# Optimization experiments

Measured on AMD Instinct MI355X. Metric: run time of the kernel, lower is better.

Reference implementation:

```python
import jax, jax.numpy as jnp
import numpy as np

X_DIM, Z_DIM, H, B, T = 257, 16, 128, 256, 512


def _p(key, shape, scale=0.05):
    return jax.random.normal(key, shape, jnp.float32) * scale


def setup_inputs() -> dict:
    key = jax.random.key(0)
    ks = jax.random.split(key, 16)
    z4 = jnp.zeros((4 * H,), jnp.float32)
    return {
        "x": jax.random.uniform(ks[0], (B, X_DIM, T), jnp.float32),
        "eps": jax.random.normal(ks[1], (T, B, Z_DIM), jnp.float32),
        # rnn_g_x: backward LSTM over x
        "Wih_gx": _p(ks[2], (4 * H, X_DIM)), "Whh_gx": _p(ks[3], (4 * H, H)),
        "bih_gx": z4, "bhh_gx": z4,
        # rnn_g_z: forward LSTM cell over sampled z
        "Wih_gz": _p(ks[4], (4 * H, Z_DIM)), "Whh_gz": _p(ks[5], (4 * H, H)),
        "bih_gz": z4, "bhh_gz": z4,
        # mlp_inference (one dense layer, tanh) + heads
        "W0": _p(ks[6], (H, 2 * H)), "b0": jnp.zeros((H,), jnp.float32),
        "Wm": _p(ks[7], (Z_DIM, H)), "bm": jnp.zeros((Z_DIM,), jnp.float32),
        "Wv": _p(ks[8], (Z_DIM, H)), "bv": jnp.zeros((Z_DIM,), jnp.float32),
        # decoder rnn_h + gen_logvar
        "Wih_h": _p(ks[9], (4 * H, Z_DIM)), "Whh_h": _p(ks[10], (4 * H, H)),
        "bih_h": z4, "bhh_h": z4,
        "Wy": _p(ks[11], (X_DIM, H)), "by": jnp.zeros((X_DIM,), jnp.float32),
    }


def _lstm(xs, Wih, Whh, b, reverse=False):
    # xs: (T, B, in); single-layer LSTM, PyTorch gate order i,f,g,o
    Bn, Hd = xs.shape[1], Whh.shape[1]

    def step(carry, x_t):
        h, c = carry
        g = x_t @ Wih.T + h @ Whh.T + b
        i, f, gg, o = jnp.split(g, 4, axis=-1)
        c = jax.nn.sigmoid(f) * c + jax.nn.sigmoid(i) * jnp.tanh(gg)
        h = jax.nn.sigmoid(o) * jnp.tanh(c)
        return (h, c), h

    init = (jnp.zeros((Bn, Hd), xs.dtype), jnp.zeros((Bn, Hd), xs.dtype))
    _, hs = jax.lax.scan(step, init, xs, reverse=reverse)
    return hs


def reference(x, eps, Wih_gx, Whh_gx, bih_gx, bhh_gx,
              Wih_gz, Whh_gz, bih_gz, bhh_gz,
              W0, b0, Wm, bm, Wv, bv,
              Wih_h, Whh_h, bih_h, bhh_h, Wy, by):
    xt = jnp.transpose(x, (2, 0, 1))  # (T, B, x_dim)
    # g_x = flip(LSTM(flip(x))) == backward-direction LSTM
    g_x = _lstm(xt, Wih_gx, Whh_gx, bih_gx + bhh_gx, reverse=True)
    bz = bih_gz + bhh_gz
    Hz = Whh_gz.shape[1]

    def inf_step(carry, inp):
        g_z, c_z = carry  # hidden of rnn_g_z BEFORE seeing current z
        gx_t, eps_t = inp
        h = jnp.tanh(jnp.concatenate([gx_t, g_z], axis=-1) @ W0.T + b0)
        mean = h @ Wm.T + bm
        logvar = h @ Wv.T + bv
        z_t = eps_t * jnp.exp(0.5 * logvar) + mean  # reparameterize
        # one LSTM-cell step of rnn_g_z on z_t (used at next timestep)
        g = z_t @ Wih_gz.T + g_z @ Whh_gz.T + bz
        i, f, gg, o = jnp.split(g, 4, axis=-1)
        c_z = jax.nn.sigmoid(f) * c_z + jax.nn.sigmoid(i) * jnp.tanh(gg)
        g_z = jax.nn.sigmoid(o) * jnp.tanh(c_z)
        return (g_z, c_z), (mean, logvar, z_t)

    Bn = xt.shape[1]
    init = (jnp.zeros((Bn, Hz), x.dtype), jnp.zeros((Bn, Hz), x.dtype))
    _, (mean, logvar, z) = jax.lax.scan(inf_step, init, (g_x, eps))
    # generation
    hdec = _lstm(z, Wih_h, Whh_h, bih_h + bhh_h)
    y = jnp.exp(hdec @ Wy.T + by)  # (T, B, x_dim)
    perm = lambda a: jnp.transpose(a, (1, 2, 0))  # -> (B, dim, T)
    return perm(y), perm(mean), perm(logvar), perm(z)
```

## Files before the change

### kernel.cpp

```cpp
#include <hip/hip_runtime.h>
#include <stdint.h>

#define T_SEQ 512
#define BATCH 256
#define HID   128
#define G4    512
#define XD    257
#define ZD    16

__device__ __forceinline__ float bf2f(uint16_t u) {
  union { uint32_t i; float f; } v; v.i = ((uint32_t)u) << 16; return v.f;
}
__device__ __forceinline__ uint16_t f2bf(float f) {
  union { float f; uint32_t i; } v; v.f = f;
  uint32_t r = v.i + 0x7fffu + ((v.i >> 16) & 1u);
  return (uint16_t)(r >> 16);
}
__device__ __forceinline__ float sigf(float x) { return 1.0f / (1.0f + __expf(-x)); }
__device__ __forceinline__ float tanhfast(float x) { return 2.0f / (1.0f + __expf(-2.0f * x)) - 1.0f; }
__device__ __forceinline__ float gate_act(float pre, bool isg) {
  float s = isg ? (-2.0f * pre) : (-pre);
  float r = 1.0f / (1.0f + __expf(s));
  return isg ? (2.0f * r - 1.0f) : r;
}

__global__ void k_prep(const float* __restrict__ Wih_gx, const float* __restrict__ Wy,
                       float* __restrict__ wT, float* __restrict__ wyT) {
  int idx = blockIdx.x * 256 + threadIdx.x;
  const int N1 = XD * G4;
  const int N2 = HID * XD;
  if (idx < N1) {
    int j = idx & (G4 - 1), d = idx >> 9;
    wT[idx] = Wih_gx[j * XD + d];
  } else if (idx < N1 + N2) {
    int i2 = idx - N1;
    int u = i2 / XD, d = i2 % XD;
    wyT[i2] = Wy[d * HID + u];
  }
}

__global__ __launch_bounds__(256) void k_proj(
    const float* __restrict__ x, const float* __restrict__ wT,
    const float* __restrict__ bih, const float* __restrict__ bhh,
    uint16_t* __restrict__ px) {
  __shared__ uint16_t xs[XD * 66];
  int tid = threadIdx.x;
  int t0 = blockIdx.x * 64, b = blockIdx.y;
  int lane = tid & 63;
  {
    int t = tid & 63, d0 = tid >> 6;
    for (int d = d0; d < XD; d += 4)
      xs[d * 66 + t] = f2bf(x[((size_t)b * XD + d) * T_SEQ + t0 + t]);
  }
  __syncthreads();
  int w = __builtin_amdgcn_readfirstlane(tid >> 6);
  for (int p = 0; p < 8; ++p) {
    int j0 = w * 128 + p * 16;
    float acc[16];
#pragma unroll
    for (int i = 0; i < 16; ++i) acc[i] = bih[j0 + i] + bhh[j0 + i];
    for (int d = 0; d < XD; ++d) {
      float xv = bf2f(xs[d * 66 + lane]);
      const float* wrow = wT + (size_t)d * G4 + j0;
#pragma unroll
      for (int i = 0; i < 16; ++i) acc[i] = fmaf(wrow[i], xv, acc[i]);
    }
    size_t base = ((size_t)(t0 + lane) * BATCH + b) * G4 + j0;
    uint32_t pk[8];
#pragma unroll
    for (int i = 0; i < 8; ++i)
      pk[i] = (uint32_t)f2bf(acc[2 * i]) | ((uint32_t)f2bf(acc[2 * i + 1]) << 16);
    uint4* dst = (uint4*)(px + base);
    dst[0] = make_uint4(pk[0], pk[1], pk[2], pk[3]);
    dst[1] = make_uint4(pk[4], pk[5], pk[6], pk[7]);
  }
}

__global__ __launch_bounds__(512, 2) void k_lstm_gx(
    const uint16_t* __restrict__ px, const float* __restrict__ Whh,
    uint16_t* __restrict__ gx) {
  __shared__ __align__(16) float hl[2][HID];
  int tid = threadIdx.x, b = blockIdx.x;
  int u = tid >> 2, g = tid & 3;
  int j = g * HID + u;
  float wr[HID];
#pragma unroll
  for (int k = 0; k < HID; ++k) wr[k] = Whh[(size_t)j * HID + k];
  if (tid < HID) hl[0][tid] = 0.0f;
  float c = 0.0f;
  int cur = 0;
  int ql = (tid & 63) & ~3;
  bool isg = (g == 2);
  uint16_t pcur = px[((size_t)(T_SEQ - 1) * BATCH + b) * G4 + j];
  __syncthreads();
  for (int t = T_SEQ - 1; t >= 0; --t) {
    int tn = t > 0 ? t - 1 : 0;
    uint16_t pnext = px[((size_t)tn * BATCH + b) * G4 + j];
    float pre = bf2f(pcur);
    const float4* h4 = (const float4*)hl[cur];
#pragma unroll
    for (int k4 = 0; k4 < HID / 4; ++k4) {
      float4 h = h4[k4];
      pre = fmaf(wr[4 * k4 + 0], h.x, pre);
      pre = fmaf(wr[4 * k4 + 1], h.y, pre);
      pre = fmaf(wr[4 * k4 + 2], h.z, pre);
      pre = fmaf(wr[4 * k4 + 3], h.w, pre);
    }
    float act = gate_act(pre, isg);
    float af = __shfl(act, ql + 1);
    float ag = __shfl(act, ql + 2);
    float ao = __shfl(act, ql + 3);
    if (g == 0) {
      c = af * c + act * ag;
      float h = ao * tanhfast(c);
      hl[cur ^ 1][u] = h;
      gx[((size_t)t * BATCH + b) * HID + u] = f2bf(h);
    }
    cur ^= 1;
    pcur = pnext;
    __syncthreads();
  }
}

__global__ __launch_bounds__(512, 2) void k_inf(
    const uint16_t* __restrict__ gx, const float* __restrict__ eps,
    const float* __restrict__ Wih_gz, const float* __restrict__ Whh_gz,
    const float* __restrict__ bih_gz, const float* __restrict__ bhh_gz,
    const float* __restrict__ W0, const float* __restrict__ b0,
    const float* __restrict__ Wm, const float* __restrict__ bm,
    const float* __restrict__ Wv, const float* __restrict__ bv,
    float* __restrict__ zbuf, float* __restrict__ out_mean,
    float* __restrict__ out_logvar, float* __restrict__ out_z) {
  __shared__ float wgzT2[ZD * 512];
  __shared__ __align__(16) float gxl[HID];
  __shared__ __align__(16) float gzl[2][HID];
  __shared__ __align__(16) float hvec[HID];
  __shared__ __align__(16) float zl[ZD];
  int tid = threadIdx.x, b = blockIdx.x;
  int u = tid >> 2, g = tid & 3;
  int j = g * HID + u;
#pragma unroll
  for (int k = 0; k < ZD; ++k) wgzT2[k * 512 + tid] = Wih_gz[(size_t)j * ZD + k];
  float wzr[HID];
#pragma unroll
  for (int k = 0; k < HID; ++k) wzr[k] = Whh_gz[(size_t)j * HID + k];
  float bzr = bih_gz[j] + bhh_gz[j];
  float w0r[64];
#pragma unroll
  for (int i = 0; i < 64; ++i) w0r[i] = W0[(size_t)u * 256 + g * 64 + i];
  float b0r = b0[u];
  int o = tid >> 5, lo = tid & 31;
  float wmr[8];
  {
    const float* Wsel = (lo < 16) ? (Wm + (size_t)o * HID + lo * 8)
                                  : (Wv + (size_t)o * HID + (lo - 16) * 8);
#pragma unroll
    for (int i = 0; i < 8; ++i) wmr[i] = Wsel[i];
  }
  float bmr = bm[o], bvr = bv[o];
  float czr = 0.0f;
  int cur = 0;
  int ql = (tid & 63) & ~3;
  bool isg = (g == 2);
  if (tid < HID) {
    gzl[0][tid] = 0.0f;
    gxl[tid] = bf2f(gx[(size_t)b * HID + tid]);
  }
  float epcur = (lo == 0) ? eps[(size_t)b * ZD + o] : 0.0f;
  __syncthreads();
  for (int t = 0; t < T_SEQ; ++t) {
    int tn = (t < T_SEQ - 1) ? t + 1 : t;
    float gxnext = (tid < HID) ? bf2f(gx[((size_t)tn * BATCH + b) * HID + tid]) : 0.0f;
    float epnext = (lo == 0) ? eps[((size_t)tn * BATCH + b) * ZD + o] : 0.0f;
    {
      const float4* src = (const float4*)((g < 2) ? (gxl + g * 64) : (gzl[cur] + (g - 2) * 64));
      float p = 0.0f;
#pragma unroll
      for (int i4 = 0; i4 < 16; ++i4) {
        float4 v = src[i4];
        p = fmaf(w0r[4 * i4 + 0], v.x, p);
        p = fmaf(w0r[4 * i4 + 1], v.y, p);
        p = fmaf(w0r[4 * i4 + 2], v.z, p);
        p = fmaf(w0r[4 * i4 + 3], v.w, p);
      }
      p += __shfl_xor(p, 1);
      p += __shfl_xor(p, 2);
      if (g == 0) hvec[u] = tanhfast(p + b0r);
    }
    __syncthreads();
    {
      int hbase = (lo & 15) * 8;
      const float4* hh = (const float4*)(hvec + hbase);
      float4 h0 = hh[0], h1 = hh[1];
      float p = wmr[0] * h0.x + wmr[1] * h0.y + wmr[2] * h0.z + wmr[3] * h0.w +
                wmr[4] * h1.x + wmr[5] * h1.y + wmr[6] * h1.z + wmr[7] * h1.w;
      p += __shfl_xor(p, 1);
      p += __shfl_xor(p, 2);
      p += __shfl_xor(p, 4);
      p += __shfl_xor(p, 8);
      float other = __shfl_xor(p, 16);
      if (lo == 0) {
        float mean = p + bmr;
        float lv = other + bvr;
        float zv = epcur * __expf(0.5f * lv) + mean;
        zl[o] = zv;
        out_mean[((size_t)b * ZD + o) * T_SEQ + t] = mean;
        out_logvar[((size_t)b * ZD + o) * T_SEQ + t] = lv;
        out_z[((size_t)b * ZD + o) * T_SEQ + t] = zv;
        zbuf[((size_t)t * BATCH + b) * ZD + o] = zv;
      }
    }
    __syncthreads();
    {
      float pre = bzr;
#pragma unroll
      for (int k = 0; k < ZD; ++k) pre = fmaf(zl[k], wgzT2[k * 512 + tid], pre);
      const float4* g4 = (const float4*)gzl[cur];
#pragma unroll
      for (int k4 = 0; k4 < HID / 4; ++k4) {
        float4 hv = g4[k4];
        pre = fmaf(wzr[4 * k4 + 0], hv.x, pre);
        pre = fmaf(wzr[4 * k4 + 1], hv.y, pre);
        pre = fmaf(wzr[4 * k4 + 2], hv.z, pre);
        pre = fmaf(wzr[4 * k4 + 3], hv.w, pre);
      }
      float act = gate_act(pre, isg);
      float af = __shfl(act, ql + 1);
      float ag = __shfl(act, ql + 2);
      float ao = __shfl(act, ql + 3);
      if (g == 0) {
        czr = af * czr + act * ag;
        gzl[cur ^ 1][u] = ao * tanhfast(czr);
      }
      if (tid < HID) gxl[tid] = gxnext;
    }
    epcur = epnext;
    cur ^= 1;
    __syncthreads();
  }
}

__global__ __launch_bounds__(512, 2) void k_dec(
    const float* __restrict__ zbuf, const float* __restrict__ Wih_h,
    const float* __restrict__ Whh_h, const float* __restrict__ bih,
    const float* __restrict__ bhh, uint16_t* __restrict__ hdec) {
  __shared__ float wihT2[ZD * 512];
  __shared__ __align__(16) float hl[2][HID];
  __shared__ float zls[2][ZD];
  int tid = threadIdx.x, b = blockIdx.x;
  int u = tid >> 2, g = tid & 3;
  int j = g * HID + u;
#pragma unroll
  for (int k = 0; k < ZD; ++k) wihT2[k * 512 + tid] = Wih_h[(size_t)j * ZD + k];
  float wr[HID];
#pragma unroll
  for (int k = 0; k < HID; ++k) wr[k] = Whh_h[(size_t)j * HID + k];
  float bz = bih[j] + bhh[j];
  if (tid < HID) hl[0][tid] = 0.0f;
  if (tid < ZD) zls[0][tid] = zbuf[(size_t)b * ZD + tid];
  float c = 0.0f;
  int cur = 0;
  int ql = (tid & 63) & ~3;
  bool isg = (g == 2);
  __syncthreads();
  for (int t = 0; t < T_SEQ; ++t) {
    int tn = (t < T_SEQ - 1) ? t + 1 : t;
    float znext = (tid < ZD) ? zbuf[((size_t)tn * BATCH + b) * ZD + tid] : 0.0f;
    float pre = bz;
#pragma unroll
    for (int k = 0; k < ZD; ++k) pre = fmaf(zls[cur][k], wihT2[k * 512 + tid], pre);
    const float4* h4 = (const float4*)hl[cur];
#pragma unroll
    for (int k4 = 0; k4 < HID / 4; ++k4) {
      float4 h = h4[k4];
      pre = fmaf(wr[4 * k4 + 0], h.x, pre);
      pre = fmaf(wr[4 * k4 + 1], h.y, pre);
      pre = fmaf(wr[4 * k4 + 2], h.z, pre);
      pre = fmaf(wr[4 * k4 + 3], h.w, pre);
    }
    float act = gate_act(pre, isg);
    float af = __shfl(act, ql + 1);
    float ag = __shfl(act, ql + 2);
    float ao = __shfl(act, ql + 3);
    if (g == 0) {
      c = af * c + act * ag;
      float h = ao * tanhfast(c);
      hl[cur ^ 1][u] = h;
      hdec[((size_t)t * BATCH + b) * HID + u] = f2bf(h);
    }
    if (tid < ZD) zls[cur ^ 1][tid] = znext;
    cur ^= 1;
    __syncthreads();
  }
}

__global__ __launch_bounds__(256) void k_y(
    const uint16_t* __restrict__ hdec, const float* __restrict__ wyT,
    const float* __restrict__ by, float* __restrict__ out_y) {
  __shared__ __align__(16) float hl[HID * 65];
  int tid = threadIdx.x;
  int t0 = blockIdx.x * 64, b = blockIdx.y;
  {
    int uu = tid & 127, tg = tid >> 7;
    for (int tt = tg; tt < 64; tt += 2)
      hl[uu * 65 + tt] = bf2f(hdec[((size_t)(t0 + tt) * BATCH + b) * HID + uu]);
  }
  __syncthreads();
  int w = __builtin_amdgcn_readfirstlane(tid >> 6);
  int lane = tid & 63;
  for (int p = 0; p < 4; ++p) {
    int d0 = w * 16 + p * 64;
    float acc[16];
#pragma unroll
    for (int i = 0; i < 16; ++i) acc[i] = by[d0 + i];
    for (int uu = 0; uu < HID; ++uu) {
      float hv = hl[uu * 65 + lane];
      const float* wrow = wyT + (size_t)uu * XD + d0;
#pragma unroll
      for (int i = 0; i < 16; ++i) acc[i] = fmaf(wrow[i], hv, acc[i]);
    }
#pragma unroll
    for (int i = 0; i < 16; ++i)
      out_y[((size_t)b * XD + d0 + i) * T_SEQ + t0 + lane] = __expf(acc[i]);
  }
  if (w == 0) {
    float acc = by[256];
    for (int uu = 0; uu < HID; ++uu)
      acc = fmaf(wyT[(size_t)uu * XD + 256], hl[uu * 65 + lane], acc);
    out_y[((size_t)b * XD + 256) * T_SEQ + t0 + lane] = __expf(acc);
  }
}

extern "C" void kernel_launch(void* const* d_in, const int* in_sizes, int n_in,
                              void* d_out, int out_size, void* d_ws, size_t ws_size,
                              hipStream_t stream) {
  const float* x      = (const float*)d_in[0];
  const float* eps    = (const float*)d_in[1];
  const float* Wih_gx = (const float*)d_in[2];
  const float* Whh_gx = (const float*)d_in[3];
  const float* bih_gx = (const float*)d_in[4];
  const float* bhh_gx = (const float*)d_in[5];
  const float* Wih_gz = (const float*)d_in[6];
  const float* Whh_gz = (const float*)d_in[7];
  const float* bih_gz = (const float*)d_in[8];
  const float* bhh_gz = (const float*)d_in[9];
  const float* W0     = (const float*)d_in[10];
  const float* b0     = (const float*)d_in[11];
  const float* Wm     = (const float*)d_in[12];
  const float* bm     = (const float*)d_in[13];
  const float* Wv     = (const float*)d_in[14];
  const float* bv     = (const float*)d_in[15];
  const float* Wih_h  = (const float*)d_in[16];
  const float* Whh_h  = (const float*)d_in[17];
  const float* bih_h  = (const float*)d_in[18];
  const float* bhh_h  = (const float*)d_in[19];
  const float* Wy     = (const float*)d_in[20];
  const float* by     = (const float*)d_in[21];

  char* ws = (char*)d_ws;
  float*    wT   = (float*)(ws + 0);
  float*    wyT  = (float*)(ws + 526336);
  uint16_t* px   = (uint16_t*)(ws + (1u << 20));
  uint16_t* gx   = (uint16_t*)(ws + 135266304);
  float*    zbuf = (float*)(ws + 168820736);
  uint16_t* hdec = (uint16_t*)(ws + 177209344);

  float* out_y      = (float*)d_out;
  float* out_mean   = out_y + (size_t)BATCH * XD * T_SEQ;
  float* out_logvar = out_mean + (size_t)BATCH * ZD * T_SEQ;
  float* out_z      = out_logvar + (size_t)BATCH * ZD * T_SEQ;

  k_prep<<<dim3(643), dim3(256), 0, stream>>>(Wih_gx, Wy, wT, wyT);
  k_proj<<<dim3(8, 256), dim3(256), 0, stream>>>(x, wT, bih_gx, bhh_gx, px);
  k_lstm_gx<<<dim3(256), dim3(512), 0, stream>>>(px, Whh_gx, gx);
  k_inf<<<dim3(256), dim3(512), 0, stream>>>(gx, eps, Wih_gz, Whh_gz, bih_gz, bhh_gz,
                                             W0, b0, Wm, bm, Wv, bv,
                                             zbuf, out_mean, out_logvar, out_z);
  k_dec<<<dim3(256), dim3(512), 0, stream>>>(zbuf, Wih_h, Whh_h, bih_h, bhh_h, hdec);
  k_y<<<dim3(8, 256), dim3(256), 0, stream>>>(hdec, wyT, by, out_y);
}
```

Baseline: 4.266 ms.

## Split recurrent matvecs over quad lanes with DPP reductions and swizzled LDS reads

The three recurrent kernels now split the K dimension across the 4 lanes of a quad. Each lane computes partial sums for all four gates over a 32-element slice, with XOR-rotated float4 reads to avoid LDS bank conflicts. A DPP quad transpose-reduce then combines the partials. This cuts LDS traffic per step from a full 128-element broadcast read per thread to 32 elements, and replaces ds_bpermute shuffles with DPP and ds_swizzle. The input projection weights move from LDS into registers, and the W0 matvec in k_inf is re-tiled with lane-group reductions and a padded hvec layout, at the cost of extra selects and register pressure.

```diff
diff --git a/kernel.cpp b/kernel.cpp
--- a/kernel.cpp
+++ b/kernel.cpp
@@ -16,12 +16,31 @@
   uint32_t r = v.i + 0x7fffu + ((v.i >> 16) & 1u);
   return (uint16_t)(r >> 16);
 }
-__device__ __forceinline__ float sigf(float x) { return 1.0f / (1.0f + __expf(-x)); }
 __device__ __forceinline__ float tanhfast(float x) { return 2.0f / (1.0f + __expf(-2.0f * x)) - 1.0f; }
 __device__ __forceinline__ float gate_act(float pre, bool isg) {
   float s = isg ? (-2.0f * pre) : (-pre);
   float r = 1.0f / (1.0f + __expf(s));
   return isg ? (2.0f * r - 1.0f) : r;
+}
+
+template <int C>
+__device__ __forceinline__ float dppq(float x) {
+  return __int_as_float(__builtin_amdgcn_mov_dpp(__float_as_int(x), C, 0xF, 0xF, true));
+}
+template <int O>
+__device__ __forceinline__ float swzx(float x) {
+  return __int_as_float(__builtin_amdgcn_ds_swizzle(__float_as_int(x), O));
+}
+
+__device__ __forceinline__ float quad_reduce4(float a0, float a1, float a2, float a3, int g) {
+  bool lb = (g & 1) != 0;
+  float rl = dppq<0xB1>(lb ? a0 : a1);
+  float rh = dppq<0xB1>(lb ? a2 : a3);
+  float bl = (lb ? a1 : a0) + rl;
+  float bh = (lb ? a3 : a2) + rh;
+  bool hb = (g & 2) != 0;
+  float r2 = dppq<0x4E>(hb ? bl : bh);
+  return (hb ? bh : bl) + r2;
 }
 
 __global__ void k_prep(const float* __restrict__ Wih_gx, const float* __restrict__ Wy,
@@ -79,37 +98,49 @@
 __global__ __launch_bounds__(512, 2) void k_lstm_gx(
     const uint16_t* __restrict__ px, const float* __restrict__ Whh,
     uint16_t* __restrict__ gx) {
-  __shared__ __align__(16) float hl[2][HID];
+  __shared__ __align__(128) float hl[2][HID];
   int tid = threadIdx.x, b = blockIdx.x;
   int u = tid >> 2, g = tid & 3;
   int j = g * HID + u;
-  float wr[HID];
-#pragma unroll
-  for (int k = 0; k < HID; ++k) wr[k] = Whh[(size_t)j * HID + k];
+  int rot = g << 1, hbase = g << 3;
+  float wA[4][32];
+#pragma unroll
+  for (int q = 0; q < 4; ++q)
+#pragma unroll
+    for (int n = 0; n < 8; ++n) {
+      int i = n ^ rot;
+      float4 wv = *(const float4*)(Whh + ((size_t)(q * HID + u)) * HID + g * 32 + i * 4);
+      wA[q][4 * n + 0] = wv.x; wA[q][4 * n + 1] = wv.y;
+      wA[q][4 * n + 2] = wv.z; wA[q][4 * n + 3] = wv.w;
+    }
   if (tid < HID) hl[0][tid] = 0.0f;
   float c = 0.0f;
   int cur = 0;
-  int ql = (tid & 63) & ~3;
   bool isg = (g == 2);
   uint16_t pcur = px[((size_t)(T_SEQ - 1) * BATCH + b) * G4 + j];
   __syncthreads();
   for (int t = T_SEQ - 1; t >= 0; --t) {
     int tn = t > 0 ? t - 1 : 0;
     uint16_t pnext = px[((size_t)tn * BATCH + b) * G4 + j];
-    float pre = bf2f(pcur);
     const float4* h4 = (const float4*)hl[cur];
-#pragma unroll
-    for (int k4 = 0; k4 < HID / 4; ++k4) {
-      float4 h = h4[k4];
-      pre = fmaf(wr[4 * k4 + 0], h.x, pre);
-      pre = fmaf(wr[4 * k4 + 1], h.y, pre);
-      pre = fmaf(wr[4 * k4 + 2], h.z, pre);
-      pre = fmaf(wr[4 * k4 + 3], h.w, pre);
-    }
+    float a0 = 0.f, a1 = 0.f, a2 = 0.f, a3 = 0.f;
+#pragma unroll
+    for (int n = 0; n < 8; ++n) {
+      float4 hv = h4[hbase + (n ^ rot)];
+      a0 = fmaf(wA[0][4 * n + 0], hv.x, a0); a0 = fmaf(wA[0][4 * n + 1], hv.y, a0);
+      a0 = fmaf(wA[0][4 * n + 2], hv.z, a0); a0 = fmaf(wA[0][4 * n + 3], hv.w, a0);
+      a1 = fmaf(wA[1][4 * n + 0], hv.x, a1); a1 = fmaf(wA[1][4 * n + 1], hv.y, a1);
+      a1 = fmaf(wA[1][4 * n + 2], hv.z, a1); a1 = fmaf(wA[1][4 * n + 3], hv.w, a1);
+      a2 = fmaf(wA[2][4 * n + 0], hv.x, a2); a2 = fmaf(wA[2][4 * n + 1], hv.y, a2);
+      a2 = fmaf(wA[2][4 * n + 2], hv.z, a2); a2 = fmaf(wA[2][4 * n + 3], hv.w, a2);
+      a3 = fmaf(wA[3][4 * n + 0], hv.x, a3); a3 = fmaf(wA[3][4 * n + 1], hv.y, a3);
+      a3 = fmaf(wA[3][4 * n + 2], hv.z, a3); a3 = fmaf(wA[3][4 * n + 3], hv.w, a3);
+    }
+    float pre = quad_reduce4(a0, a1, a2, a3, g) + bf2f(pcur);
     float act = gate_act(pre, isg);
-    float af = __shfl(act, ql + 1);
-    float ag = __shfl(act, ql + 2);
-    float ao = __shfl(act, ql + 3);
+    float af = dppq<0x55>(act);
+    float ag = dppq<0xAA>(act);
+    float ao = dppq<0xFF>(act);
     if (g == 0) {
       c = af * c + act * ag;
       float h = ao * tanhfast(c);
@@ -131,36 +162,50 @@
     const float* __restrict__ Wv, const float* __restrict__ bv,
     float* __restrict__ zbuf, float* __restrict__ out_mean,
     float* __restrict__ out_logvar, float* __restrict__ out_z) {
-  __shared__ float wgzT2[ZD * 512];
-  __shared__ __align__(16) float gxl[HID];
-  __shared__ __align__(16) float gzl[2][HID];
-  __shared__ __align__(16) float hvec[HID];
-  __shared__ __align__(16) float zl[ZD];
+  __shared__ __align__(128) float gxl[HID];
+  __shared__ __align__(128) float gzl[2][HID];
+  __shared__ __align__(128) float hvec[16 * 12];
+  __shared__ __align__(128) float zl[ZD];
   int tid = threadIdx.x, b = blockIdx.x;
   int u = tid >> 2, g = tid & 3;
   int j = g * HID + u;
-#pragma unroll
-  for (int k = 0; k < ZD; ++k) wgzT2[k * 512 + tid] = Wih_gz[(size_t)j * ZD + k];
-  float wzr[HID];
-#pragma unroll
-  for (int k = 0; k < HID; ++k) wzr[k] = Whh_gz[(size_t)j * HID + k];
+  int rot = g << 1, hbase = g << 3;
+  float wA[4][32];
+  float4 wz[4];
+#pragma unroll
+  for (int q = 0; q < 4; ++q) {
+#pragma unroll
+    for (int n = 0; n < 8; ++n) {
+      int i = n ^ rot;
+      float4 wv = *(const float4*)(Whh_gz + ((size_t)(q * HID + u)) * HID + g * 32 + i * 4);
+      wA[q][4 * n + 0] = wv.x; wA[q][4 * n + 1] = wv.y;
+      wA[q][4 * n + 2] = wv.z; wA[q][4 * n + 3] = wv.w;
+    }
+    wz[q] = *(const float4*)(Wih_gz + (size_t)(q * HID + u) * ZD + g * 4);
+  }
   float bzr = bih_gz[j] + bhh_gz[j];
-  float w0r[64];
-#pragma unroll
-  for (int i = 0; i < 64; ++i) w0r[i] = W0[(size_t)u * 256 + g * 64 + i];
-  float b0r = b0[u];
+  int sB = tid & 7, uB = (tid >> 3) << 1;
+  float w0a[32], w0b[32];
+#pragma unroll
+  for (int n = 0; n < 8; ++n) {
+    int i = n ^ sB;
+    float4 va = *(const float4*)(W0 + (size_t)uB * 256 + sB * 32 + i * 4);
+    float4 vb = *(const float4*)(W0 + (size_t)(uB + 1) * 256 + sB * 32 + i * 4);
+    w0a[4 * n + 0] = va.x; w0a[4 * n + 1] = va.y; w0a[4 * n + 2] = va.z; w0a[4 * n + 3] = va.w;
+    w0b[4 * n + 0] = vb.x; w0b[4 * n + 1] = vb.y; w0b[4 * n + 2] = vb.z; w0b[4 * n + 3] = vb.w;
+  }
+  float b0a = b0[uB], b0b = b0[uB + 1];
   int o = tid >> 5, lo = tid & 31;
   float wmr[8];
   {
-    const float* Wsel = (lo < 16) ? (Wm + (size_t)o * HID + lo * 8)
-                                  : (Wv + (size_t)o * HID + (lo - 16) * 8);
+    const float* Wsel = (lo < 16) ? (Wm + (size_t)o * HID + (lo & 15) * 8)
+                                  : (Wv + (size_t)o * HID + (lo & 15) * 8);
 #pragma unroll
     for (int i = 0; i < 8; ++i) wmr[i] = Wsel[i];
   }
   float bmr = bm[o], bvr = bv[o];
   float czr = 0.0f;
   int cur = 0;
-  int ql = (tid & 63) & ~3;
   bool isg = (g == 2);
   if (tid < HID) {
     gzl[0][tid] = 0.0f;
@@ -173,32 +218,37 @@
     float gxnext = (tid < HID) ? bf2f(gx[((size_t)tn * BATCH + b) * HID + tid]) : 0.0f;
     float epnext = (lo == 0) ? eps[((size_t)tn * BATCH + b) * ZD + o] : 0.0f;
     {
-      const float4* src = (const float4*)((g < 2) ? (gxl + g * 64) : (gzl[cur] + (g - 2) * 64));
-      float p = 0.0f;
-#pragma unroll
-      for (int i4 = 0; i4 < 16; ++i4) {
-        float4 v = src[i4];
-        p = fmaf(w0r[4 * i4 + 0], v.x, p);
-        p = fmaf(w0r[4 * i4 + 1], v.y, p);
-        p = fmaf(w0r[4 * i4 + 2], v.z, p);
-        p = fmaf(w0r[4 * i4 + 3], v.w, p);
+      const float4* seg = (sB < 4) ? ((const float4*)gxl + (sB << 3))
+                                   : ((const float4*)(gzl[cur]) + ((sB - 4) << 3));
+      float pa = 0.f, pb = 0.f;
+#pragma unroll
+      for (int n = 0; n < 8; ++n) {
+        float4 v = seg[n ^ sB];
+        pa = fmaf(w0a[4 * n + 0], v.x, pa); pa = fmaf(w0a[4 * n + 1], v.y, pa);
+        pa = fmaf(w0a[4 * n + 2], v.z, pa); pa = fmaf(w0a[4 * n + 3], v.w, pa);
+        pb = fmaf(w0b[4 * n + 0], v.x, pb); pb = fmaf(w0b[4 * n + 1], v.y, pb);
+        pb = fmaf(w0b[4 * n + 2], v.z, pb); pb = fmaf(w0b[4 * n + 3], v.w, pb);
       }
-      p += __shfl_xor(p, 1);
-      p += __shfl_xor(p, 2);
-      if (g == 0) hvec[u] = tanhfast(p + b0r);
+      pa += dppq<0xB1>(pa); pa += dppq<0x4E>(pa); pa += swzx<0x101F>(pa);
+      pb += dppq<0xB1>(pb); pb += dppq<0x4E>(pb); pb += swzx<0x101F>(pb);
+      if (sB == 0) {
+        hvec[((uB >> 3) * 12) + (uB & 7)] = tanhfast(pa + b0a);
+        int u1 = uB + 1;
+        hvec[((u1 >> 3) * 12) + (u1 & 7)] = tanhfast(pb + b0b);
+      }
     }
     __syncthreads();
     {
-      int hbase = (lo & 15) * 8;
-      const float4* hh = (const float4*)(hvec + hbase);
+      int m = lo & 15;
+      const float4* hh = (const float4*)(hvec + m * 12);
       float4 h0 = hh[0], h1 = hh[1];
       float p = wmr[0] * h0.x + wmr[1] * h0.y + wmr[2] * h0.z + wmr[3] * h0.w +
                 wmr[4] * h1.x + wmr[5] * h1.y + wmr[6] * h1.z + wmr[7] * h1.w;
-      p += __shfl_xor(p, 1);
-      p += __shfl_xor(p, 2);
-      p += __shfl_xor(p, 4);
-      p += __shfl_xor(p, 8);
-      float other = __shfl_xor(p, 16);
+      p += dppq<0xB1>(p);
+      p += dppq<0x4E>(p);
+      p += swzx<0x101F>(p);
+      p += swzx<0x201F>(p);
+      float other = swzx<0x401F>(p);
       if (lo == 0) {
         float mean = p + bmr;
         float lv = other + bvr;
@@ -212,22 +262,33 @@
     }
     __syncthreads();
     {
-      float pre = bzr;
-#pragma unroll
-      for (int k = 0; k < ZD; ++k) pre = fmaf(zl[k], wgzT2[k * 512 + tid], pre);
-      const float4* g4 = (const float4*)gzl[cur];
-#pragma unroll
-      for (int k4 = 0; k4 < HID / 4; ++k4) {
-        float4 hv = g4[k4];
-        pre = fmaf(wzr[4 * k4 + 0], hv.x, pre);
-        pre = fmaf(wzr[4 * k4 + 1], hv.y, pre);
-        pre = fmaf(wzr[4 * k4 + 2], hv.z, pre);
-        pre = fmaf(wzr[4 * k4 + 3], hv.w, pre);
+      float4 zv = ((const float4*)zl)[g];
+      float a0 = wz[0].x * zv.x; a0 = fmaf(wz[0].y, zv.y, a0);
+      a0 = fmaf(wz[0].z, zv.z, a0); a0 = fmaf(wz[0].w, zv.w, a0);
+      float a1 = wz[1].x * zv.x; a1 = fmaf(wz[1].y, zv.y, a1);
+      a1 = fmaf(wz[1].z, zv.z, a1); a1 = fmaf(wz[1].w, zv.w, a1);
+      float a2 = wz[2].x * zv.x; a2 = fmaf(wz[2].y, zv.y, a2);
+      a2 = fmaf(wz[2].z, zv.z, a2); a2 = fmaf(wz[2].w, zv.w, a2);
+      float a3 = wz[3].x * zv.x; a3 = fmaf(wz[3].y, zv.y, a3);
+      a3 = fmaf(wz[3].z, zv.z, a3); a3 = fmaf(wz[3].w, zv.w, a3);
+      const float4* h4 = (const float4*)gzl[cur];
+#pragma unroll
+      for (int n = 0; n < 8; ++n) {
+        float4 hv = h4[hbase + (n ^ rot)];
+        a0 = fmaf(wA[0][4 * n + 0], hv.x, a0); a0 = fmaf(wA[0][4 * n + 1], hv.y, a0);
+        a0 = fmaf(wA[0][4 * n + 2], hv.z, a0); a0 = fmaf(wA[0][4 * n + 3], hv.w, a0);
+        a1 = fmaf(wA[1][4 * n + 0], hv.x, a1); a1 = fmaf(wA[1][4 * n + 1], hv.y, a1);
+        a1 = fmaf(wA[1][4 * n + 2], hv.z, a1); a1 = fmaf(wA[1][4 * n + 3], hv.w, a1);
+        a2 = fmaf(wA[2][4 * n + 0], hv.x, a2); a2 = fmaf(wA[2][4 * n + 1], hv.y, a2);
+        a2 = fmaf(wA[2][4 * n + 2], hv.z, a2); a2 = fmaf(wA[2][4 * n + 3], hv.w, a2);
+        a3 = fmaf(wA[3][4 * n + 0], hv.x, a3); a3 = fmaf(wA[3][4 * n + 1], hv.y, a3);
+        a3 = fmaf(wA[3][4 * n + 2], hv.z, a3); a3 = fmaf(wA[3][4 * n + 3], hv.w, a3);
       }
+      float pre = quad_reduce4(a0, a1, a2, a3, g) + bzr;
       float act = gate_act(pre, isg);
-      float af = __shfl(act, ql + 1);
-      float ag = __shfl(act, ql + 2);
-      float ao = __shfl(act, ql + 3);
+      float af = dppq<0x55>(act);
+      float ag = dppq<0xAA>(act);
+      float ao = dppq<0xFF>(act);
       if (g == 0) {
         czr = af * czr + act * ag;
         gzl[cur ^ 1][u] = ao * tanhfast(czr);
@@ -244,44 +305,62 @@
     const float* __restrict__ zbuf, const float* __restrict__ Wih_h,
     const float* __restrict__ Whh_h, const float* __restrict__ bih,
     const float* __restrict__ bhh, uint16_t* __restrict__ hdec) {
-  __shared__ float wihT2[ZD * 512];
-  __shared__ __align__(16) float hl[2][HID];
-  __shared__ float zls[2][ZD];
+  __shared__ __align__(128) float hl[2][HID];
+  __shared__ __align__(128) float zls[2][ZD];
   int tid = threadIdx.x, b = blockIdx.x;
   int u = tid >> 2, g = tid & 3;
   int j = g * HID + u;
-#pragma unroll
-  for (int k = 0; k < ZD; ++k) wihT2[k * 512 + tid] = Wih_h[(size_t)j * ZD + k];
-  float wr[HID];
-#pragma unroll
-  for (int k = 0; k < HID; ++k) wr[k] = Whh_h[(size_t)j * HID + k];
+  int rot = g << 1, hbase = g << 3;
+  float wA[4][32];
+  float4 wz[4];
+#pragma unroll
+  for (int q = 0; q < 4; ++q) {
+#pragma unroll
+    for (int n = 0; n < 8; ++n) {
+      int i = n ^ rot;
+      float4 wv = *(const float4*)(Whh_h + ((size_t)(q * HID + u)) * HID + g * 32 + i * 4);
+      wA[q][4 * n + 0] = wv.x; wA[q][4 * n + 1] = wv.y;
+      wA[q][4 * n + 2] = wv.z; wA[q][4 * n + 3] = wv.w;
+    }
+    wz[q] = *(const float4*)(Wih_h + (size_t)(q * HID + u) * ZD + g * 4);
+  }
   float bz = bih[j] + bhh[j];
   if (tid < HID) hl[0][tid] = 0.0f;
   if (tid < ZD) zls[0][tid] = zbuf[(size_t)b * ZD + tid];
   float c = 0.0f;
   int cur = 0;
-  int ql = (tid & 63) & ~3;
   bool isg = (g == 2);
   __syncthreads();
   for (int t = 0; t < T_SEQ; ++t) {
     int tn = (t < T_SEQ - 1) ? t + 1 : t;
     float znext = (tid < ZD) ? zbuf[((size_t)tn * BATCH + b) * ZD + tid] : 0.0f;
-    float pre = bz;
-#pragma unroll
-    for (int k = 0; k < ZD; ++k) pre = fmaf(zls[cur][k], wihT2[k * 512 + tid], pre);
+    float4 zv = ((const float4*)zls[cur])[g];
+    float a0 = wz[0].x * zv.x; a0 = fmaf(wz[0].y, zv.y, a0);
+    a0 = fmaf(wz[0].z, zv.z, a0); a0 = fmaf(wz[0].w, zv.w, a0);
+    float a1 = wz[1].x * zv.x; a1 = fmaf(wz[1].y, zv.y, a1);
+    a1 = fmaf(wz[1].z, zv.z, a1); a1 = fmaf(wz[1].w, zv.w, a1);
+    float a2 = wz[2].x * zv.x; a2 = fmaf(wz[2].y, zv.y, a2);
+    a2 = fmaf(wz[2].z, zv.z, a2); a2 = fmaf(wz[2].w, zv.w, a2);
+    float a3 = wz[3].x * zv.x; a3 = fmaf(wz[3].y, zv.y, a3);
+    a3 = fmaf(wz[3].z, zv.z, a3); a3 = fmaf(wz[3].w, zv.w, a3);
     const float4* h4 = (const float4*)hl[cur];
 #pragma unroll
-    for (int k4 = 0; k4 < HID / 4; ++k4) {
-      float4 h = h4[k4];
-      pre = fmaf(wr[4 * k4 + 0], h.x, pre);
-      pre = fmaf(wr[4 * k4 + 1], h.y, pre);
-      pre = fmaf(wr[4 * k4 + 2], h.z, pre);
-      pre = fmaf(wr[4 * k4 + 3], h.w, pre);
-    }
+    for (int n = 0; n < 8; ++n) {
+      float4 hv = h4[hbase + (n ^ rot)];
+      a0 = fmaf(wA[0][4 * n + 0], hv.x, a0); a0 = fmaf(wA[0][4 * n + 1], hv.y, a0);
+      a0 = fmaf(wA[0][4 * n + 2], hv.z, a0); a0 = fmaf(wA[0][4 * n + 3], hv.w, a0);
+      a1 = fmaf(wA[1][4 * n + 0], hv.x, a1); a1 = fmaf(wA[1][4 * n + 1], hv.y, a1);
+      a1 = fmaf(wA[1][4 * n + 2], hv.z, a1); a1 = fmaf(wA[1][4 * n + 3], hv.w, a1);
+      a2 = fmaf(wA[2][4 * n + 0], hv.x, a2); a2 = fmaf(wA[2][4 * n + 1], hv.y, a2);
+      a2 = fmaf(wA[2][4 * n + 2], hv.z, a2); a2 = fmaf(wA[2][4 * n + 3], hv.w, a2);
+      a3 = fmaf(wA[3][4 * n + 0], hv.x, a3); a3 = fmaf(wA[3][4 * n + 1], hv.y, a3);
+      a3 = fmaf(wA[3][4 * n + 2], hv.z, a3); a3 = fmaf(wA[3][4 * n + 3], hv.w, a3);
+    }
+    float pre = quad_reduce4(a0, a1, a2, a3, g) + bz;
     float act = gate_act(pre, isg);
-    float af = __shfl(act, ql + 1);
-    float ag = __shfl(act, ql + 2);
-    float ao = __shfl(act, ql + 3);
+    float af = dppq<0x55>(act);
+    float ag = dppq<0xAA>(act);
+    float ao = dppq<0xFF>(act);
     if (g == 0) {
       c = af * c + act * ag;
       float h = ao * tanhfast(c);
```

Result: faster. 3.515 ms (-17.6%).
